# Performance work log

Measured on AMD Instinct MI355X. Metric: run time of the kernel, lower is better.

Reference implementation:

```python
import jax, jax.numpy as jnp
import numpy as np

# Config matching init_kwargs (single TP rank: local heads == total heads)
HID = 1024
NH = 16      # query heads
NKV = 4      # kv heads (GQA)
HD = 64      # head_dim
B = 2
S = 2048
SCALE = 1.0 / HD ** 0.5


def setup_inputs() -> dict:
    key = jax.random.key(0)
    k1, k2, k3 = jax.random.split(key, 3)
    qkv_out = (NH + 2 * NKV) * HD  # 1536
    return {
        "hidden_states": jax.random.normal(k1, (B, S, HID), dtype=jnp.float32),
        "W_qkv": jax.random.normal(k2, (HID, qkv_out), dtype=jnp.float32) * 0.02,
        "W_o": jax.random.normal(k3, (HID, HID), dtype=jnp.float32) * 0.02,
    }


def reference(hidden_states, W_qkv, W_o):
    b, s, _ = hidden_states.shape
    rep = NH // NKV  # GQA repeat factor (repeat_interleave: q head h uses kv group h // rep)

    qkv = hidden_states @ W_qkv  # [B, S, (NH+2*NKV)*HD]
    q, k, v = jnp.split(qkv, [NH * HD, (NH + NKV) * HD], axis=-1)

    # [B, heads, S, HD]
    q = q.reshape(b, s, NH, HD).transpose(0, 2, 1, 3)
    k = k.reshape(b, s, NKV, HD).transpose(0, 2, 1, 3)
    v = v.reshape(b, s, NKV, HD).transpose(0, 2, 1, 3)

    # Group query heads by shared kv head instead of repeat_interleaving K/V in memory.
    qg = q.reshape(b, NKV, rep, s, HD)  # head h = g*rep + r  <=>  kv group g = h // rep
    scores = jnp.einsum("bgrqd,bgkd->bgrqk", qg, k) * SCALE  # [B, NKV, rep, S, S]

    # Causal mask (prefill path: kv_cache is None, seq_len > 1)
    causal = jnp.triu(jnp.ones((s, s), dtype=bool), k=1)
    scores = jnp.where(causal, jnp.finfo(scores.dtype).min, scores)

    attn = jax.nn.softmax(scores, axis=-1)
    out = jnp.einsum("bgrqk,bgkd->bgrqd", attn, v)  # [B, NKV, rep, S, HD]
    out = out.reshape(b, NH, s, HD).transpose(0, 2, 1, 3).reshape(b, s, NH * HD)
    return out @ W_o  # [B, S, HID]
```

## Files before the change

### kernel.cpp

```cpp
#include <hip/hip_runtime.h>
#include <stdint.h>

using u16 = unsigned short;
using u32 = unsigned int;

typedef __attribute__((ext_vector_type(8))) short short8;
typedef __attribute__((ext_vector_type(4))) float f32x4;
typedef __attribute__((ext_vector_type(16))) float f32x16;

__device__ __forceinline__ u16 f2bf(float f) {
  u32 u = __builtin_bit_cast(u32, f);
  u = (u + 0x7fffu + ((u >> 16) & 1u)) >> 16;
  return (u16)u;
}

__device__ __forceinline__ u32 cvtpk(float lo, float hi) {
  u32 r;
  asm("v_cvt_pk_bf16_f32 %0, %1, %2" : "=v"(r) : "v"(lo), "v"(hi));
  return r;
}

__device__ __forceinline__ short8 ld16(const u16* p) {
  uint4 v = *(const uint4*)p;
  union { uint4 u; short8 s; } c; c.u = v; return c.s;
}

__device__ __forceinline__ void gload_lds16(const void* g, void* l) {
  __builtin_amdgcn_global_load_lds(
      (const __attribute__((address_space(1))) void*)g,
      (__attribute__((address_space(3))) void*)l, 16, 0, 0);
}

__device__ __forceinline__ f32x16 mfma32(short8 a, short8 b, f32x16 c) {
  return __builtin_amdgcn_mfma_f32_32x32x16_bf16(a, b, c, 0, 0, 0);
}

__global__ __launch_bounds__(256) void k_f32_to_bf16(const float* __restrict__ in,
                                                     u16* __restrict__ out, int n4) {
  int i = blockIdx.x * 256 + threadIdx.x;
  if (i >= n4) return;
  float4 v = ((const float4*)in)[i];
  ushort4 o;
  o.x = f2bf(v.x); o.y = f2bf(v.y); o.z = f2bf(v.z); o.w = f2bf(v.w);
  ((ushort4*)out)[i] = o;
}

__global__ __launch_bounds__(256) void k_transpose_bf16(const float* __restrict__ in,
                                                        u16* __restrict__ out, int R, int C) {
  __shared__ float tile[32][33];
  int c0 = blockIdx.x * 32, r0 = blockIdx.y * 32;
  int tx = threadIdx.x & 31, ty = threadIdx.x >> 5;
#pragma unroll
  for (int i = 0; i < 4; ++i) {
    int r = ty + 8 * i;
    tile[r][tx] = in[(size_t)(r0 + r) * C + c0 + tx];
  }
  __syncthreads();
#pragma unroll
  for (int i = 0; i < 4; ++i) {
    int r = ty + 8 * i;
    out[(size_t)(c0 + r) * R + r0 + tx] = f2bf(tile[tx][r]);
  }
}

template <int EPI>
__global__ __launch_bounds__(256, 2) void k_gemm(
    const u16* __restrict__ A, const u16* __restrict__ BT, int M, int N, int K,
    u16* __restrict__ qb, u16* __restrict__ kb, u16* __restrict__ vbT,
    float* __restrict__ out) {
  __shared__ __align__(16) u16 As[128 * 64];
  __shared__ __align__(16) u16 Bs[128 * 64];
  const int t = threadIdx.x;
  const int l = t & 63;
  const int wid = t >> 6;
  const int wr = wid >> 1, wc = wid & 1;
  const int lr = l & 15, lg = l >> 4;
  const int ntile = N >> 7;
  const int mt = blockIdx.x / ntile, nt = blockIdx.x % ntile;
  const int m0 = mt << 7, n0 = nt << 7;

  f32x4 zero = {0.f, 0.f, 0.f, 0.f};
  f32x4 acc[4][4];
#pragma unroll
  for (int i = 0; i < 4; ++i)
#pragma unroll
    for (int j = 0; j < 4; ++j) acc[i][j] = zero;

  const u16* Ab = A + (size_t)m0 * K;
  const u16* Bb = BT + (size_t)n0 * K;
  const int nkt = K >> 6;

  for (int kt = 0; kt < nkt; ++kt) {
    const u16* Ak = Ab + kt * 64;
    const u16* Bk = Bb + kt * 64;
#pragma unroll
    for (int i = 0; i < 4; ++i) {
      int o16 = i * 256 + t;
      int row = o16 >> 3, c = o16 & 7;
      int sc = c ^ (row & 7);
      gload_lds16(Ak + (size_t)row * K + sc * 8, &As[o16 * 8]);
    }
#pragma unroll
    for (int i = 0; i < 4; ++i) {
      int o16 = i * 256 + t;
      int row = o16 >> 3, c = o16 & 7;
      int sc = c ^ (row & 7);
      gload_lds16(Bk + (size_t)row * K + sc * 8, &Bs[o16 * 8]);
    }
    __syncthreads();
#pragma unroll
    for (int ks = 0; ks < 2; ++ks) {
      short8 a[4], b[4];
#pragma unroll
      for (int mi = 0; mi < 4; ++mi) {
        int row = wr * 64 + mi * 16 + lr;
        int c = (ks * 4 + lg) ^ (row & 7);
        a[mi] = ld16(&As[(row * 8 + c) * 8]);
      }
#pragma unroll
      for (int ni = 0; ni < 4; ++ni) {
        int row = wc * 64 + ni * 16 + lr;
        int c = (ks * 4 + lg) ^ (row & 7);
        b[ni] = ld16(&Bs[(row * 8 + c) * 8]);
      }
#pragma unroll
      for (int mi = 0; mi < 4; ++mi)
#pragma unroll
        for (int ni = 0; ni < 4; ++ni)
          acc[mi][ni] = __builtin_amdgcn_mfma_f32_16x16x32_bf16(a[mi], b[ni], acc[mi][ni], 0, 0, 0);
    }
    __syncthreads();
  }

#pragma unroll
  for (int mi = 0; mi < 4; ++mi) {
#pragma unroll
    for (int ni = 0; ni < 4; ++ni) {
#pragma unroll
      for (int r = 0; r < 4; ++r) {
        float v = acc[mi][ni][r];
        int m = m0 + wr * 64 + mi * 16 + 4 * lg + r;
        int n = n0 + wc * 64 + ni * 16 + lr;
        if (EPI == 0) {
          int bb = m >> 11, s = m & 2047;
          int tau = s >> 5, i32e = s & 31;
          if (n < 1024) {
            int h = n >> 6, d = n & 63;
            int kc = d >> 4, hi2 = (d >> 3) & 1, e = d & 7;
            qb[((size_t)(bb * 16 + h)) * 131072 +
               (size_t)((tau * 4 + kc) * 64 + (hi2 << 5 | i32e)) * 8 + e] = f2bf(v * 0.18033688f);
          } else if (n < 1280) {
            int g = (n - 1024) >> 6, d = n & 63;
            int kc = d >> 4, hi2 = (d >> 3) & 1, e = d & 7;
            kb[((size_t)(bb * 4 + g)) * 131072 +
               (size_t)((tau * 4 + kc) * 64 + (hi2 << 5 | i32e)) * 8 + e] = f2bf(v);
          } else {
            int g = (n - 1280) >> 6, dT = n & 63;
            int c = (s >> 4) & 1, hi2 = (s >> 3) & 1, e = s & 7;
            int dd = dT >> 5, i32v = dT & 31;
            vbT[((size_t)(bb * 4 + g)) * 131072 +
                (size_t)(((tau * 2 + dd) * 2 + c) * 64 + (hi2 << 5 | i32v)) * 8 + e] = f2bf(v);
          }
        } else {
          out[(size_t)m * N + n] = v;
        }
      }
    }
  }
}

__global__ __launch_bounds__(256, 2) void k_attn(const u16* __restrict__ qbuf,
                                                 const u16* __restrict__ kbuf,
                                                 const u16* __restrict__ vbuf,
                                                 u16* __restrict__ attn) {
  const int t = threadIdx.x;
  const int l = t & 63, wid = t >> 6;
  const int i32 = l & 31, hi = l >> 5;
  const int bh = blockIdx.x >> 4;
  const int t16 = blockIdx.x & 15;
  const int b = bh >> 4, h = bh & 15, g = h >> 2;
  const int qt = (wid == 0) ? t16 : (wid == 1) ? 31 - t16 : (wid == 2) ? 32 + t16 : 63 - t16;
  const int q0 = qt * 32;
  const int nblk = (q0 >> 6) + 1;

  const u16* qp = qbuf + ((size_t)(b * 16 + h)) * 131072;
  const u16* kp = kbuf + ((size_t)(b * 4 + g)) * 131072;
  const u16* vp = vbuf + ((size_t)(b * 4 + g)) * 131072;

  short8 qf[4];
#pragma unroll
  for (int kc = 0; kc < 4; ++kc)
    qf[kc] = ld16(qp + ((size_t)((q0 >> 5) * 4 + kc) * 64 + l) * 8);

  f32x16 z16 = {0.f, 0.f, 0.f, 0.f, 0.f, 0.f, 0.f, 0.f,
                0.f, 0.f, 0.f, 0.f, 0.f, 0.f, 0.f, 0.f};
  f32x16 o[2];
  o[0] = z16; o[1] = z16;
  float mrun = -1e30f, lsum = 0.f;

  short8 kA[2][4], kB[2][4];

  auto LOADK = [&](short8(&kf)[2][4], int kv0) {
#pragma unroll
    for (int mf = 0; mf < 2; ++mf)
#pragma unroll
      for (int kc = 0; kc < 4; ++kc)
        kf[mf][kc] = ld16(kp + ((size_t)((((kv0 >> 5) + mf) * 4 + kc)) * 64 + l) * 8);
  };

  auto PROCESS = [&](short8(&kf)[2][4], short8(&kn)[2][4], bool pref, int kv0, bool last) {
    short8 vf[2][2][2];
#pragma unroll
    for (int mf = 0; mf < 2; ++mf)
#pragma unroll
      for (int dd = 0; dd < 2; ++dd)
#pragma unroll
        for (int c = 0; c < 2; ++c)
          vf[dd][mf][c] = ld16(vp + ((size_t)((((kv0 >> 5) + mf) * 2 + dd) * 2 + c) * 64 + l) * 8);

    f32x16 sc[2];
    __builtin_amdgcn_s_setprio(1);
    sc[0] = mfma32(kf[0][0], qf[0], z16);
    sc[1] = mfma32(kf[1][0], qf[0], z16);
#pragma unroll
    for (int kc = 1; kc < 4; ++kc) {
      sc[0] = mfma32(kf[0][kc], qf[kc], sc[0]);
      sc[1] = mfma32(kf[1][kc], qf[kc], sc[1]);
    }
    __builtin_amdgcn_s_setprio(0);

    if (pref) LOADK(kn, kv0 + 64);

    if (last) {
      const int iloc = (q0 - kv0) + i32;
#pragma unroll
      for (int mf = 0; mf < 2; ++mf)
#pragma unroll
        for (int R = 0; R < 16; ++R) {
          int j = 32 * mf + (R & 3) + 8 * (R >> 2) + 4 * hi;
          if (j > iloc) sc[mf][R] = -1e30f;
        }
    }

    float mq[8];
#pragma unroll
    for (int k = 0; k < 8; ++k) {
      int mf = k >> 2, b4 = (k & 3) * 4;
      mq[k] = fmaxf(fmaxf(sc[mf][b4], sc[mf][b4 + 1]), fmaxf(sc[mf][b4 + 2], sc[mf][b4 + 3]));
    }
    float mx = fmaxf(fmaxf(fmaxf(mq[0], mq[1]), fmaxf(mq[2], mq[3])),
                     fmaxf(fmaxf(mq[4], mq[5]), fmaxf(mq[6], mq[7])));
    {
      u32 mu = __builtin_bit_cast(u32, mx);
      auto r = __builtin_amdgcn_permlane32_swap(mu, mu, false, false);
      mx = fmaxf(__builtin_bit_cast(float, (u32)r[0]), __builtin_bit_cast(float, (u32)r[1]));
    }
    if (!__all(mx - mrun <= 8.0f)) {
      float mnew = fmaxf(mrun, mx);
      float alpha = __builtin_amdgcn_exp2f(mrun - mnew);
      mrun = mnew;
      lsum *= alpha;
#pragma unroll
      for (int dd = 0; dd < 2; ++dd)
#pragma unroll
        for (int R = 0; R < 16; ++R) o[dd][R] *= alpha;
    }

    float s0 = 0.f, s1 = 0.f, s2 = 0.f, s3 = 0.f;
#pragma unroll
    for (int mf = 0; mf < 2; ++mf)
#pragma unroll
      for (int R = 0; R < 16; R += 4) {
        float p0 = __builtin_amdgcn_exp2f(sc[mf][R] - mrun);
        float p1 = __builtin_amdgcn_exp2f(sc[mf][R + 1] - mrun);
        float p2 = __builtin_amdgcn_exp2f(sc[mf][R + 2] - mrun);
        float p3 = __builtin_amdgcn_exp2f(sc[mf][R + 3] - mrun);
        sc[mf][R] = p0; sc[mf][R + 1] = p1; sc[mf][R + 2] = p2; sc[mf][R + 3] = p3;
        s0 += p0; s1 += p1; s2 += p2; s3 += p3;
      }
    lsum += (s0 + s1) + (s2 + s3);

    short8 pb[2][2];
#pragma unroll
    for (int mf = 0; mf < 2; ++mf)
#pragma unroll
      for (int c = 0; c < 2; ++c) {
        union { u32 w[4]; short8 s8; } U;
#pragma unroll
        for (int q = 0; q < 2; ++q) {
          u32 wa = cvtpk(sc[mf][8 * c + 2 * q], sc[mf][8 * c + 2 * q + 1]);
          u32 wb = cvtpk(sc[mf][8 * c + 4 + 2 * q], sc[mf][8 * c + 4 + 2 * q + 1]);
          auto r = __builtin_amdgcn_permlane32_swap(wa, wb, false, false);
          U.w[q] = (u32)r[0];
          U.w[2 + q] = (u32)r[1];
        }
        pb[mf][c] = U.s8;
      }

    __builtin_amdgcn_s_setprio(1);
#pragma unroll
    for (int mf = 0; mf < 2; ++mf)
#pragma unroll
      for (int c = 0; c < 2; ++c) {
        o[0] = mfma32(vf[0][mf][c], pb[mf][c], o[0]);
        o[1] = mfma32(vf[1][mf][c], pb[mf][c], o[1]);
      }
    __builtin_amdgcn_s_setprio(0);
  };

  LOADK(kA, 0);
  int kv0 = 0, blk = 0;
  while (true) {
    PROCESS(kA, kB, blk + 1 < nblk, kv0, blk == nblk - 1);
    ++blk; kv0 += 64;
    if (blk >= nblk) break;
    PROCESS(kB, kA, blk + 1 < nblk, kv0, blk == nblk - 1);
    ++blk; kv0 += 64;
    if (blk >= nblk) break;
  }

  float tot;
  {
    u32 su = __builtin_bit_cast(u32, lsum);
    auto r = __builtin_amdgcn_permlane32_swap(su, su, false, false);
    tot = __builtin_bit_cast(float, (u32)r[0]) + __builtin_bit_cast(float, (u32)r[1]);
  }
  float inv = 1.f / tot;
  u16* ao = attn + ((size_t)(b * 2048 + q0)) * 1024 + h * 64;
#pragma unroll
  for (int dd = 0; dd < 2; ++dd) {
#pragma unroll
    for (int R = 0; R < 16; R += 2) {
      int d = dd * 32 + (R & 3) + 8 * (R >> 2) + 4 * hi;
      u32 w = cvtpk(o[dd][R] * inv, o[dd][R + 1] * inv);
      *(u32*)(ao + (size_t)i32 * 1024 + d) = w;
    }
  }
}

extern "C" void kernel_launch(void* const* d_in, const int* in_sizes, int n_in,
                              void* d_out, int out_size, void* d_ws, size_t ws_size,
                              hipStream_t stream) {
  const float* hs = (const float*)d_in[0];
  const float* wqkv = (const float*)d_in[1];
  const float* wo = (const float*)d_in[2];
  float* out = (float*)d_out;
  u16* ws = (u16*)d_ws;

  u16* hsb = ws;
  u16* wqkvT = hsb + 4194304;
  u16* woT = wqkvT + 1572864;
  u16* qb = woT + 1048576;
  u16* kb = qb + 4194304;
  u16* vb = kb + 1048576;
  u16* attn = vb + 1048576;
  (void)in_sizes; (void)n_in; (void)out_size; (void)ws_size;

  k_f32_to_bf16<<<4096, 256, 0, stream>>>(hs, hsb, 1048576);
  k_transpose_bf16<<<dim3(48, 32), 256, 0, stream>>>(wqkv, wqkvT, 1024, 1536);
  k_transpose_bf16<<<dim3(32, 32), 256, 0, stream>>>(wo, woT, 1024, 1024);
  k_gemm<0><<<384, 256, 0, stream>>>(hsb, wqkvT, 4096, 1536, 1024, qb, kb, vb, nullptr);
  k_attn<<<512, 256, 0, stream>>>(qb, kb, vb, attn);
  k_gemm<1><<<256, 256, 0, stream>>>(attn, woT, 4096, 1024, 1024, nullptr, nullptr, nullptr, out);
}
```

Measured before the change: 97.22 us.

## Double-buffer GEMM LDS tiles, swizzle block order, software-pipeline QK in attention

The GEMM now keeps two LDS buffers so global-to-LDS loads for the next K tile are issued while the current tile feeds MFMA, replacing two barriers per iteration with one. Block indices are remapped in groups of 8, likely to spread neighbouring tiles across XCDs for cache locality. The attention loop is software-pipelined: the QK^T MFMAs for the next KV block run alongside the softmax and PV of the current block, and K is prefetched two blocks ahead. These changes double GEMM LDS use, which may reduce occupancy, and raise register pressure in attention.

```diff
diff --git a/kernel.cpp b/kernel.cpp
--- a/kernel.cpp
+++ b/kernel.cpp
@@ -68,15 +68,17 @@
     const u16* __restrict__ A, const u16* __restrict__ BT, int M, int N, int K,
     u16* __restrict__ qb, u16* __restrict__ kb, u16* __restrict__ vbT,
     float* __restrict__ out) {
-  __shared__ __align__(16) u16 As[128 * 64];
-  __shared__ __align__(16) u16 Bs[128 * 64];
+  __shared__ __align__(16) u16 As[2][128 * 64];
+  __shared__ __align__(16) u16 Bs[2][128 * 64];
   const int t = threadIdx.x;
   const int l = t & 63;
   const int wid = t >> 6;
   const int wr = wid >> 1, wc = wid & 1;
   const int lr = l & 15, lg = l >> 4;
+  const int cpx = (int)gridDim.x >> 3;
+  const int nb = (blockIdx.x & 7) * cpx + ((int)blockIdx.x >> 3);
   const int ntile = N >> 7;
-  const int mt = blockIdx.x / ntile, nt = blockIdx.x % ntile;
+  const int mt = nb / ntile, nt = nb % ntile;
   const int m0 = mt << 7, n0 = nt << 7;
 
   f32x4 zero = {0.f, 0.f, 0.f, 0.f};
@@ -90,7 +92,7 @@
   const u16* Bb = BT + (size_t)n0 * K;
   const int nkt = K >> 6;
 
-  for (int kt = 0; kt < nkt; ++kt) {
+  auto STAGE = [&](int kt, int bsel) {
     const u16* Ak = Ab + kt * 64;
     const u16* Bk = Bb + kt * 64;
 #pragma unroll
@@ -98,16 +100,24 @@
       int o16 = i * 256 + t;
       int row = o16 >> 3, c = o16 & 7;
       int sc = c ^ (row & 7);
-      gload_lds16(Ak + (size_t)row * K + sc * 8, &As[o16 * 8]);
+      gload_lds16(Ak + (size_t)row * K + sc * 8, &As[bsel][o16 * 8]);
     }
 #pragma unroll
     for (int i = 0; i < 4; ++i) {
       int o16 = i * 256 + t;
       int row = o16 >> 3, c = o16 & 7;
       int sc = c ^ (row & 7);
-      gload_lds16(Bk + (size_t)row * K + sc * 8, &Bs[o16 * 8]);
-    }
-    __syncthreads();
+      gload_lds16(Bk + (size_t)row * K + sc * 8, &Bs[bsel][o16 * 8]);
+    }
+  };
+
+  STAGE(0, 0);
+  asm volatile("s_waitcnt vmcnt(0)" ::: "memory");
+  __builtin_amdgcn_s_barrier();
+
+  for (int kt = 0; kt < nkt; ++kt) {
+    const int cur = kt & 1;
+    if (kt + 1 < nkt) STAGE(kt + 1, cur ^ 1);
 #pragma unroll
     for (int ks = 0; ks < 2; ++ks) {
       short8 a[4], b[4];
@@ -115,13 +125,13 @@
       for (int mi = 0; mi < 4; ++mi) {
         int row = wr * 64 + mi * 16 + lr;
         int c = (ks * 4 + lg) ^ (row & 7);
-        a[mi] = ld16(&As[(row * 8 + c) * 8]);
+        a[mi] = ld16(&As[cur][(row * 8 + c) * 8]);
       }
 #pragma unroll
       for (int ni = 0; ni < 4; ++ni) {
         int row = wc * 64 + ni * 16 + lr;
         int c = (ks * 4 + lg) ^ (row & 7);
-        b[ni] = ld16(&Bs[(row * 8 + c) * 8]);
+        b[ni] = ld16(&Bs[cur][(row * 8 + c) * 8]);
       }
 #pragma unroll
       for (int mi = 0; mi < 4; ++mi)
@@ -129,7 +139,9 @@
         for (int ni = 0; ni < 4; ++ni)
           acc[mi][ni] = __builtin_amdgcn_mfma_f32_16x16x32_bf16(a[mi], b[ni], acc[mi][ni], 0, 0, 0);
     }
-    __syncthreads();
+    asm volatile("s_waitcnt vmcnt(0)" ::: "memory");
+    __builtin_amdgcn_s_barrier();
+    asm volatile("" ::: "memory");
   }
 
 #pragma unroll
@@ -208,7 +220,16 @@
         kf[mf][kc] = ld16(kp + ((size_t)((((kv0 >> 5) + mf) * 4 + kc)) * 64 + l) * 8);
   };
 
-  auto PROCESS = [&](short8(&kf)[2][4], short8(&kn)[2][4], bool pref, int kv0, bool last) {
+  auto QK = [&](short8(&kf)[2][4]) -> f32x16 {
+    return z16;
+  };
+  (void)QK;
+
+  auto ITER = [&](f32x16(&scS)[2], f32x16(&scQ)[2], short8(&kcur)[2][4],
+                  short8(&kpre)[2][4], int n) {
+    const int kv0 = n * 64;
+    const bool last = (n == nblk - 1);
+
     short8 vf[2][2][2];
 #pragma unroll
     for (int mf = 0; mf < 2; ++mf)
@@ -218,19 +239,6 @@
         for (int c = 0; c < 2; ++c)
           vf[dd][mf][c] = ld16(vp + ((size_t)((((kv0 >> 5) + mf) * 2 + dd) * 2 + c) * 64 + l) * 8);
 
-    f32x16 sc[2];
-    __builtin_amdgcn_s_setprio(1);
-    sc[0] = mfma32(kf[0][0], qf[0], z16);
-    sc[1] = mfma32(kf[1][0], qf[0], z16);
-#pragma unroll
-    for (int kc = 1; kc < 4; ++kc) {
-      sc[0] = mfma32(kf[0][kc], qf[kc], sc[0]);
-      sc[1] = mfma32(kf[1][kc], qf[kc], sc[1]);
-    }
-    __builtin_amdgcn_s_setprio(0);
-
-    if (pref) LOADK(kn, kv0 + 64);
-
     if (last) {
       const int iloc = (q0 - kv0) + i32;
 #pragma unroll
@@ -238,7 +246,7 @@
 #pragma unroll
         for (int R = 0; R < 16; ++R) {
           int j = 32 * mf + (R & 3) + 8 * (R >> 2) + 4 * hi;
-          if (j > iloc) sc[mf][R] = -1e30f;
+          if (j > iloc) scS[mf][R] = -1e30f;
         }
     }
 
@@ -246,7 +254,7 @@
 #pragma unroll
     for (int k = 0; k < 8; ++k) {
       int mf = k >> 2, b4 = (k & 3) * 4;
-      mq[k] = fmaxf(fmaxf(sc[mf][b4], sc[mf][b4 + 1]), fmaxf(sc[mf][b4 + 2], sc[mf][b4 + 3]));
+      mq[k] = fmaxf(fmaxf(scS[mf][b4], scS[mf][b4 + 1]), fmaxf(scS[mf][b4 + 2], scS[mf][b4 + 3]));
     }
     float mx = fmaxf(fmaxf(fmaxf(mq[0], mq[1]), fmaxf(mq[2], mq[3])),
                      fmaxf(fmaxf(mq[4], mq[5]), fmaxf(mq[6], mq[7])));
@@ -266,16 +274,18 @@
         for (int R = 0; R < 16; ++R) o[dd][R] *= alpha;
     }
 
+    if (n + 2 < nblk) LOADK(kpre, kv0 + 128);
+
     float s0 = 0.f, s1 = 0.f, s2 = 0.f, s3 = 0.f;
 #pragma unroll
     for (int mf = 0; mf < 2; ++mf)
 #pragma unroll
       for (int R = 0; R < 16; R += 4) {
-        float p0 = __builtin_amdgcn_exp2f(sc[mf][R] - mrun);
-        float p1 = __builtin_amdgcn_exp2f(sc[mf][R + 1] - mrun);
-        float p2 = __builtin_amdgcn_exp2f(sc[mf][R + 2] - mrun);
-        float p3 = __builtin_amdgcn_exp2f(sc[mf][R + 3] - mrun);
-        sc[mf][R] = p0; sc[mf][R + 1] = p1; sc[mf][R + 2] = p2; sc[mf][R + 3] = p3;
+        float p0 = __builtin_amdgcn_exp2f(scS[mf][R] - mrun);
+        float p1 = __builtin_amdgcn_exp2f(scS[mf][R + 1] - mrun);
+        float p2 = __builtin_amdgcn_exp2f(scS[mf][R + 2] - mrun);
+        float p3 = __builtin_amdgcn_exp2f(scS[mf][R + 3] - mrun);
+        scS[mf][R] = p0; scS[mf][R + 1] = p1; scS[mf][R + 2] = p2; scS[mf][R + 3] = p3;
         s0 += p0; s1 += p1; s2 += p2; s3 += p3;
       }
     lsum += (s0 + s1) + (s2 + s3);
@@ -288,8 +298,8 @@
         union { u32 w[4]; short8 s8; } U;
 #pragma unroll
         for (int q = 0; q < 2; ++q) {
-          u32 wa = cvtpk(sc[mf][8 * c + 2 * q], sc[mf][8 * c + 2 * q + 1]);
-          u32 wb = cvtpk(sc[mf][8 * c + 4 + 2 * q], sc[mf][8 * c + 4 + 2 * q + 1]);
+          u32 wa = cvtpk(scS[mf][8 * c + 2 * q], scS[mf][8 * c + 2 * q + 1]);
+          u32 wb = cvtpk(scS[mf][8 * c + 4 + 2 * q], scS[mf][8 * c + 4 + 2 * q + 1]);
           auto r = __builtin_amdgcn_permlane32_swap(wa, wb, false, false);
           U.w[q] = (u32)r[0];
           U.w[2 + q] = (u32)r[1];
@@ -297,6 +307,18 @@
         pb[mf][c] = U.s8;
       }
 
+    if (n + 1 < nblk) {
+      __builtin_amdgcn_s_setprio(1);
+      scQ[0] = mfma32(kcur[0][0], qf[0], z16);
+      scQ[1] = mfma32(kcur[1][0], qf[0], z16);
+#pragma unroll
+      for (int kc = 1; kc < 4; ++kc) {
+        scQ[0] = mfma32(kcur[0][kc], qf[kc], scQ[0]);
+        scQ[1] = mfma32(kcur[1][kc], qf[kc], scQ[1]);
+      }
+      __builtin_amdgcn_s_setprio(0);
+    }
+
     __builtin_amdgcn_s_setprio(1);
 #pragma unroll
     for (int mf = 0; mf < 2; ++mf)
@@ -309,14 +331,24 @@
   };
 
   LOADK(kA, 0);
-  int kv0 = 0, blk = 0;
+  if (nblk > 1) LOADK(kB, 64);
+  f32x16 scA[2], scB[2];
+  __builtin_amdgcn_s_setprio(1);
+  scA[0] = mfma32(kA[0][0], qf[0], z16);
+  scA[1] = mfma32(kA[1][0], qf[0], z16);
+#pragma unroll
+  for (int kc = 1; kc < 4; ++kc) {
+    scA[0] = mfma32(kA[0][kc], qf[kc], scA[0]);
+    scA[1] = mfma32(kA[1][kc], qf[kc], scA[1]);
+  }
+  __builtin_amdgcn_s_setprio(0);
+
+  int n = 0;
   while (true) {
-    PROCESS(kA, kB, blk + 1 < nblk, kv0, blk == nblk - 1);
-    ++blk; kv0 += 64;
-    if (blk >= nblk) break;
-    PROCESS(kB, kA, blk + 1 < nblk, kv0, blk == nblk - 1);
-    ++blk; kv0 += 64;
-    if (blk >= nblk) break;
+    ITER(scA, scB, kB, kA, n);
+    if (++n >= nblk) break;
+    ITER(scB, scA, kA, kB, n);
+    if (++n >= nblk) break;
   }
 
   float tot;
```

New measurement: 94.83 us. 2.5% less time.

## Stage K/V tiles in shared LDS for attention and double-buffer GEMM loads

Applied to the files above, without the earlier changes.

The attention kernel now has the four waves of a block handle four consecutive 32-row query tiles of one head. The block cooperatively stages each 64-key K/V block into double-buffered LDS with global_load_lds, replacing per-wave direct global loads. This removes redundant global traffic, since four waves share one K/V stream, but adds per-block barriers and leaves waves with fewer causal blocks idle until the longest wave finishes. The GEMM gains double-buffered LDS staging that overlaps the next K-tile load with MFMA compute, plus an XCD-aware block remapping, at the cost of doubled LDS use.

```diff
diff --git a/kernel.cpp b/kernel.cpp
--- a/kernel.cpp
+++ b/kernel.cpp
@@ -21,6 +21,11 @@
 }
 
 __device__ __forceinline__ short8 ld16(const u16* p) {
+  uint4 v = *(const uint4*)p;
+  union { uint4 u; short8 s; } c; c.u = v; return c.s;
+}
+
+__device__ __forceinline__ short8 ld16s(const u16* p) {
   uint4 v = *(const uint4*)p;
   union { uint4 u; short8 s; } c; c.u = v; return c.s;
 }
@@ -68,15 +73,17 @@
     const u16* __restrict__ A, const u16* __restrict__ BT, int M, int N, int K,
     u16* __restrict__ qb, u16* __restrict__ kb, u16* __restrict__ vbT,
     float* __restrict__ out) {
-  __shared__ __align__(16) u16 As[128 * 64];
-  __shared__ __align__(16) u16 Bs[128 * 64];
+  __shared__ __align__(16) u16 As[2][128 * 64];
+  __shared__ __align__(16) u16 Bs[2][128 * 64];
   const int t = threadIdx.x;
   const int l = t & 63;
   const int wid = t >> 6;
   const int wr = wid >> 1, wc = wid & 1;
   const int lr = l & 15, lg = l >> 4;
+  const int cpx = (int)gridDim.x >> 3;
+  const int nb = (blockIdx.x & 7) * cpx + ((int)blockIdx.x >> 3);
   const int ntile = N >> 7;
-  const int mt = blockIdx.x / ntile, nt = blockIdx.x % ntile;
+  const int mt = nb / ntile, nt = nb % ntile;
   const int m0 = mt << 7, n0 = nt << 7;
 
   f32x4 zero = {0.f, 0.f, 0.f, 0.f};
@@ -90,7 +97,7 @@
   const u16* Bb = BT + (size_t)n0 * K;
   const int nkt = K >> 6;
 
-  for (int kt = 0; kt < nkt; ++kt) {
+  auto STAGE = [&](int kt, int bsel) {
     const u16* Ak = Ab + kt * 64;
     const u16* Bk = Bb + kt * 64;
 #pragma unroll
@@ -98,16 +105,24 @@
       int o16 = i * 256 + t;
       int row = o16 >> 3, c = o16 & 7;
       int sc = c ^ (row & 7);
-      gload_lds16(Ak + (size_t)row * K + sc * 8, &As[o16 * 8]);
+      gload_lds16(Ak + (size_t)row * K + sc * 8, &As[bsel][o16 * 8]);
     }
 #pragma unroll
     for (int i = 0; i < 4; ++i) {
       int o16 = i * 256 + t;
       int row = o16 >> 3, c = o16 & 7;
       int sc = c ^ (row & 7);
-      gload_lds16(Bk + (size_t)row * K + sc * 8, &Bs[o16 * 8]);
-    }
-    __syncthreads();
+      gload_lds16(Bk + (size_t)row * K + sc * 8, &Bs[bsel][o16 * 8]);
+    }
+  };
+
+  STAGE(0, 0);
+  asm volatile("s_waitcnt vmcnt(0)" ::: "memory");
+  __builtin_amdgcn_s_barrier();
+
+  for (int kt = 0; kt < nkt; ++kt) {
+    const int cur = kt & 1;
+    if (kt + 1 < nkt) STAGE(kt + 1, cur ^ 1);
 #pragma unroll
     for (int ks = 0; ks < 2; ++ks) {
       short8 a[4], b[4];
@@ -115,13 +130,13 @@
       for (int mi = 0; mi < 4; ++mi) {
         int row = wr * 64 + mi * 16 + lr;
         int c = (ks * 4 + lg) ^ (row & 7);
-        a[mi] = ld16(&As[(row * 8 + c) * 8]);
+        a[mi] = ld16(&As[cur][(row * 8 + c) * 8]);
       }
 #pragma unroll
       for (int ni = 0; ni < 4; ++ni) {
         int row = wc * 64 + ni * 16 + lr;
         int c = (ks * 4 + lg) ^ (row & 7);
-        b[ni] = ld16(&Bs[(row * 8 + c) * 8]);
+        b[ni] = ld16(&Bs[cur][(row * 8 + c) * 8]);
       }
 #pragma unroll
       for (int mi = 0; mi < 4; ++mi)
@@ -129,7 +144,9 @@
         for (int ni = 0; ni < 4; ++ni)
           acc[mi][ni] = __builtin_amdgcn_mfma_f32_16x16x32_bf16(a[mi], b[ni], acc[mi][ni], 0, 0, 0);
     }
-    __syncthreads();
+    asm volatile("s_waitcnt vmcnt(0)" ::: "memory");
+    __builtin_amdgcn_s_barrier();
+    asm volatile("" ::: "memory");
   }
 
 #pragma unroll
@@ -173,15 +190,18 @@
                                                  const u16* __restrict__ kbuf,
                                                  const u16* __restrict__ vbuf,
                                                  u16* __restrict__ attn) {
+  __shared__ __align__(16) u16 Ks[2][4096];
+  __shared__ __align__(16) u16 Vs[2][4096];
   const int t = threadIdx.x;
   const int l = t & 63, wid = t >> 6;
   const int i32 = l & 31, hi = l >> 5;
-  const int bh = blockIdx.x >> 4;
-  const int t16 = blockIdx.x & 15;
+  const int id = blockIdx.x;
+  const int bh = id >> 4;
+  const int T = (id & 15) ^ (((id >> 8) & 1) ? 15 : 0);
   const int b = bh >> 4, h = bh & 15, g = h >> 2;
-  const int qt = (wid == 0) ? t16 : (wid == 1) ? 31 - t16 : (wid == 2) ? 32 + t16 : 63 - t16;
-  const int q0 = qt * 32;
-  const int nblk = (q0 >> 6) + 1;
+  const int q0 = T * 128 + wid * 32;
+  const int nblkw = (q0 >> 6) + 1;
+  const int nmax = 2 * T + 2;
 
   const u16* qp = qbuf + ((size_t)(b * 16 + h)) * 131072;
   const u16* kp = kbuf + ((size_t)(b * 4 + g)) * 131072;
@@ -198,125 +218,130 @@
   o[0] = z16; o[1] = z16;
   float mrun = -1e30f, lsum = 0.f;
 
-  short8 kA[2][4], kB[2][4];
-
-  auto LOADK = [&](short8(&kf)[2][4], int kv0) {
-#pragma unroll
-    for (int mf = 0; mf < 2; ++mf)
-#pragma unroll
-      for (int kc = 0; kc < 4; ++kc)
-        kf[mf][kc] = ld16(kp + ((size_t)((((kv0 >> 5) + mf) * 4 + kc)) * 64 + l) * 8);
+  auto STAGE = [&](int n, int bsel) {
+    const u16* kblk = kp + (size_t)n * 4096;
+    const u16* vblk = vp + (size_t)n * 4096;
+    gload_lds16(kblk + t * 8, &Ks[bsel][t * 8]);
+    gload_lds16(kblk + (256 + t) * 8, &Ks[bsel][(256 + t) * 8]);
+    gload_lds16(vblk + t * 8, &Vs[bsel][t * 8]);
+    gload_lds16(vblk + (256 + t) * 8, &Vs[bsel][(256 + t) * 8]);
   };
 
-  auto PROCESS = [&](short8(&kf)[2][4], short8(&kn)[2][4], bool pref, int kv0, bool last) {
-    short8 vf[2][2][2];
-#pragma unroll
-    for (int mf = 0; mf < 2; ++mf)
-#pragma unroll
-      for (int dd = 0; dd < 2; ++dd)
-#pragma unroll
-        for (int c = 0; c < 2; ++c)
-          vf[dd][mf][c] = ld16(vp + ((size_t)((((kv0 >> 5) + mf) * 2 + dd) * 2 + c) * 64 + l) * 8);
-
-    f32x16 sc[2];
-    __builtin_amdgcn_s_setprio(1);
-    sc[0] = mfma32(kf[0][0], qf[0], z16);
-    sc[1] = mfma32(kf[1][0], qf[0], z16);
-#pragma unroll
-    for (int kc = 1; kc < 4; ++kc) {
-      sc[0] = mfma32(kf[0][kc], qf[kc], sc[0]);
-      sc[1] = mfma32(kf[1][kc], qf[kc], sc[1]);
-    }
-    __builtin_amdgcn_s_setprio(0);
-
-    if (pref) LOADK(kn, kv0 + 64);
-
-    if (last) {
-      const int iloc = (q0 - kv0) + i32;
-#pragma unroll
-      for (int mf = 0; mf < 2; ++mf)
-#pragma unroll
-        for (int R = 0; R < 16; ++R) {
-          int j = 32 * mf + (R & 3) + 8 * (R >> 2) + 4 * hi;
-          if (j > iloc) sc[mf][R] = -1e30f;
+  STAGE(0, 0);
+  asm volatile("s_waitcnt vmcnt(0)" ::: "memory");
+  __builtin_amdgcn_s_barrier();
+
+  int cur = 0;
+  for (int n = 0; n < nmax; ++n) {
+    if (n + 1 < nmax) STAGE(n + 1, cur ^ 1);
+    if (n < nblkw) {
+      const int kv0 = n * 64;
+      short8 kf[2][4];
+#pragma unroll
+      for (int mf = 0; mf < 2; ++mf)
+#pragma unroll
+        for (int kc = 0; kc < 4; ++kc)
+          kf[mf][kc] = ld16s(&Ks[cur][((mf * 4 + kc) * 64 + l) * 8]);
+
+      f32x16 sc[2];
+      __builtin_amdgcn_s_setprio(1);
+      sc[0] = mfma32(kf[0][0], qf[0], z16);
+      sc[1] = mfma32(kf[1][0], qf[0], z16);
+#pragma unroll
+      for (int kc = 1; kc < 4; ++kc) {
+        sc[0] = mfma32(kf[0][kc], qf[kc], sc[0]);
+        sc[1] = mfma32(kf[1][kc], qf[kc], sc[1]);
+      }
+      __builtin_amdgcn_s_setprio(0);
+
+      if (n == nblkw - 1) {
+        const int iloc = (q0 - kv0) + i32;
+#pragma unroll
+        for (int mf = 0; mf < 2; ++mf)
+#pragma unroll
+          for (int R = 0; R < 16; ++R) {
+            int j = 32 * mf + (R & 3) + 8 * (R >> 2) + 4 * hi;
+            if (j > iloc) sc[mf][R] = -1e30f;
+          }
+      }
+
+      float mq[8];
+#pragma unroll
+      for (int k = 0; k < 8; ++k) {
+        int mf = k >> 2, b4 = (k & 3) * 4;
+        mq[k] = fmaxf(fmaxf(sc[mf][b4], sc[mf][b4 + 1]), fmaxf(sc[mf][b4 + 2], sc[mf][b4 + 3]));
+      }
+      float mx = fmaxf(fmaxf(fmaxf(mq[0], mq[1]), fmaxf(mq[2], mq[3])),
+                       fmaxf(fmaxf(mq[4], mq[5]), fmaxf(mq[6], mq[7])));
+      {
+        u32 mu = __builtin_bit_cast(u32, mx);
+        auto r = __builtin_amdgcn_permlane32_swap(mu, mu, false, false);
+        mx = fmaxf(__builtin_bit_cast(float, (u32)r[0]), __builtin_bit_cast(float, (u32)r[1]));
+      }
+      if (!__all(mx - mrun <= 8.0f)) {
+        float mnew = fmaxf(mrun, mx);
+        float alpha = __builtin_amdgcn_exp2f(mrun - mnew);
+        mrun = mnew;
+        lsum *= alpha;
+#pragma unroll
+        for (int dd = 0; dd < 2; ++dd)
+#pragma unroll
+          for (int R = 0; R < 16; ++R) o[dd][R] *= alpha;
+      }
+
+      float s0 = 0.f, s1 = 0.f, s2 = 0.f, s3 = 0.f;
+#pragma unroll
+      for (int mf = 0; mf < 2; ++mf)
+#pragma unroll
+        for (int R = 0; R < 16; R += 4) {
+          float p0 = __builtin_amdgcn_exp2f(sc[mf][R] - mrun);
+          float p1 = __builtin_amdgcn_exp2f(sc[mf][R + 1] - mrun);
+          float p2 = __builtin_amdgcn_exp2f(sc[mf][R + 2] - mrun);
+          float p3 = __builtin_amdgcn_exp2f(sc[mf][R + 3] - mrun);
+          sc[mf][R] = p0; sc[mf][R + 1] = p1; sc[mf][R + 2] = p2; sc[mf][R + 3] = p3;
+          s0 += p0; s1 += p1; s2 += p2; s3 += p3;
         }
-    }
-
-    float mq[8];
-#pragma unroll
-    for (int k = 0; k < 8; ++k) {
-      int mf = k >> 2, b4 = (k & 3) * 4;
-      mq[k] = fmaxf(fmaxf(sc[mf][b4], sc[mf][b4 + 1]), fmaxf(sc[mf][b4 + 2], sc[mf][b4 + 3]));
-    }
-    float mx = fmaxf(fmaxf(fmaxf(mq[0], mq[1]), fmaxf(mq[2], mq[3])),
-                     fmaxf(fmaxf(mq[4], mq[5]), fmaxf(mq[6], mq[7])));
-    {
-      u32 mu = __builtin_bit_cast(u32, mx);
-      auto r = __builtin_amdgcn_permlane32_swap(mu, mu, false, false);
-      mx = fmaxf(__builtin_bit_cast(float, (u32)r[0]), __builtin_bit_cast(float, (u32)r[1]));
-    }
-    if (!__all(mx - mrun <= 8.0f)) {
-      float mnew = fmaxf(mrun, mx);
-      float alpha = __builtin_amdgcn_exp2f(mrun - mnew);
-      mrun = mnew;
-      lsum *= alpha;
-#pragma unroll
-      for (int dd = 0; dd < 2; ++dd)
-#pragma unroll
-        for (int R = 0; R < 16; ++R) o[dd][R] *= alpha;
-    }
-
-    float s0 = 0.f, s1 = 0.f, s2 = 0.f, s3 = 0.f;
-#pragma unroll
-    for (int mf = 0; mf < 2; ++mf)
-#pragma unroll
-      for (int R = 0; R < 16; R += 4) {
-        float p0 = __builtin_amdgcn_exp2f(sc[mf][R] - mrun);
-        float p1 = __builtin_amdgcn_exp2f(sc[mf][R + 1] - mrun);
-        float p2 = __builtin_amdgcn_exp2f(sc[mf][R + 2] - mrun);
-        float p3 = __builtin_amdgcn_exp2f(sc[mf][R + 3] - mrun);
-        sc[mf][R] = p0; sc[mf][R + 1] = p1; sc[mf][R + 2] = p2; sc[mf][R + 3] = p3;
-        s0 += p0; s1 += p1; s2 += p2; s3 += p3;
-      }
-    lsum += (s0 + s1) + (s2 + s3);
-
-    short8 pb[2][2];
-#pragma unroll
-    for (int mf = 0; mf < 2; ++mf)
-#pragma unroll
-      for (int c = 0; c < 2; ++c) {
-        union { u32 w[4]; short8 s8; } U;
-#pragma unroll
-        for (int q = 0; q < 2; ++q) {
-          u32 wa = cvtpk(sc[mf][8 * c + 2 * q], sc[mf][8 * c + 2 * q + 1]);
-          u32 wb = cvtpk(sc[mf][8 * c + 4 + 2 * q], sc[mf][8 * c + 4 + 2 * q + 1]);
-          auto r = __builtin_amdgcn_permlane32_swap(wa, wb, false, false);
-          U.w[q] = (u32)r[0];
-          U.w[2 + q] = (u32)r[1];
+      lsum += (s0 + s1) + (s2 + s3);
+
+      short8 pb[2][2];
+#pragma unroll
+      for (int mf = 0; mf < 2; ++mf)
+#pragma unroll
+        for (int c = 0; c < 2; ++c) {
+          union { u32 w[4]; short8 s8; } U;
+#pragma unroll
+          for (int q = 0; q < 2; ++q) {
+            u32 wa = cvtpk(sc[mf][8 * c + 2 * q], sc[mf][8 * c + 2 * q + 1]);
+            u32 wb = cvtpk(sc[mf][8 * c + 4 + 2 * q], sc[mf][8 * c + 4 + 2 * q + 1]);
+            auto r = __builtin_amdgcn_permlane32_swap(wa, wb, false, false);
+            U.w[q] = (u32)r[0];
+            U.w[2 + q] = (u32)r[1];
+          }
+          pb[mf][c] = U.s8;
         }
-        pb[mf][c] = U.s8;
-      }
-
-    __builtin_amdgcn_s_setprio(1);
-#pragma unroll
-    for (int mf = 0; mf < 2; ++mf)
-#pragma unroll
-      for (int c = 0; c < 2; ++c) {
-        o[0] = mfma32(vf[0][mf][c], pb[mf][c], o[0]);
-        o[1] = mfma32(vf[1][mf][c], pb[mf][c], o[1]);
-      }
-    __builtin_amdgcn_s_setprio(0);
-  };
-
-  LOADK(kA, 0);
-  int kv0 = 0, blk = 0;
-  while (true) {
-    PROCESS(kA, kB, blk + 1 < nblk, kv0, blk == nblk - 1);
-    ++blk; kv0 += 64;
-    if (blk >= nblk) break;
-    PROCESS(kB, kA, blk + 1 < nblk, kv0, blk == nblk - 1);
-    ++blk; kv0 += 64;
-    if (blk >= nblk) break;
+
+      short8 vf[2][2][2];
+#pragma unroll
+      for (int mf = 0; mf < 2; ++mf)
+#pragma unroll
+        for (int dd = 0; dd < 2; ++dd)
+#pragma unroll
+          for (int c = 0; c < 2; ++c)
+            vf[dd][mf][c] = ld16s(&Vs[cur][((4 * mf + 2 * dd + c) * 64 + l) * 8]);
+
+      __builtin_amdgcn_s_setprio(1);
+#pragma unroll
+      for (int mf = 0; mf < 2; ++mf)
+#pragma unroll
+        for (int c = 0; c < 2; ++c) {
+          o[0] = mfma32(vf[0][mf][c], pb[mf][c], o[0]);
+          o[1] = mfma32(vf[1][mf][c], pb[mf][c], o[1]);
+        }
+      __builtin_amdgcn_s_setprio(0);
+    }
+    asm volatile("s_waitcnt vmcnt(0)" ::: "memory");
+    __builtin_amdgcn_s_barrier();
+    cur ^= 1;
   }
 
   float tot;
```

Result: slower. 101.0 us (+3.8%).
